# Kernel tuning notes

Hardware: AMD Instinct MI355X
Metric: run time of the kernel (lower is better)

Reference implementation:

```python
import jax, jax.numpy as jnp
import numpy as np

D_IN, D_H, D_OUT = 1024, 1024, 1024
D_MOE = 4096
N_EXPERTS = 8
TOP_K = 2


def setup_inputs() -> dict:
    key = jax.random.key(0)
    ks = jax.random.split(key, 10)
    s = lambda d: 1.0 / np.sqrt(d)
    x = jax.random.normal(ks[0], (2, 2048, D_IN), dtype=jnp.float32)
    W_in = jax.random.normal(ks[1], (D_IN, D_H), dtype=jnp.float32) * s(D_IN)
    b_in = jnp.zeros((D_H,), jnp.float32)
    W_gate = jax.random.normal(ks[2], (D_H, N_EXPERTS), dtype=jnp.float32) * s(D_H)
    b_gate = jnp.zeros((N_EXPERTS,), jnp.float32)
    W1 = jax.random.normal(ks[3], (N_EXPERTS, D_H, D_MOE), dtype=jnp.float32) * s(D_H)
    b1 = jnp.zeros((N_EXPERTS, D_MOE), jnp.float32)
    W2 = jax.random.normal(ks[4], (N_EXPERTS, D_MOE, D_H), dtype=jnp.float32) * s(D_MOE)
    b2 = jnp.zeros((N_EXPERTS, D_H), jnp.float32)
    W_out = jax.random.normal(ks[5], (D_H, D_OUT), dtype=jnp.float32) * s(D_H)
    b_out = jnp.zeros((D_OUT,), jnp.float32)
    return {"x": x, "W_in": W_in, "b_in": b_in, "W_gate": W_gate, "b_gate": b_gate,
            "W1": W1, "b1": b1, "W2": W2, "b2": b2, "W_out": W_out, "b_out": b_out}


def reference(x, W_in, b_in, W_gate, b_gate, W1, b1, W2, b2, W_out, b_out):
    B, S, _ = x.shape
    h = x @ W_in + b_in                       # [B,S,D_H]
    t = h.reshape(B * S, -1)                  # tokens [N,D_H]

    # --- top-k softmax gating ---
    logits = t @ W_gate + b_gate              # [N,E]
    probs = jax.nn.softmax(logits, axis=-1)
    topv, topi = jax.lax.top_k(probs, TOP_K)  # [N,k]
    topv = topv / jnp.sum(topv, axis=-1, keepdims=True)
    # dense routing weights [N,E] (zeros for unselected experts)
    route = jnp.zeros_like(probs).at[jnp.arange(t.shape[0])[:, None], topi].set(topv)

    # --- expert MLPs (dense all-expert compute, weighted combine) ---
    mid = jax.nn.relu(jnp.einsum('nd,edh->neh', t, W1) + b1)   # [N,E,D_MOE]
    eout = jnp.einsum('neh,ehd->ned', mid, W2) + b2            # [N,E,D_H]
    moe_out = jnp.einsum('ne,ned->nd', route, eout)            # [N,D_H]

    out = moe_out.reshape(B, S, -1) @ W_out + b_out            # [B,S,D_OUT]
    return out
```

## Files before the change

kernel.cpp:

```cpp
#include <hip/hip_runtime.h>
#include <hip/hip_bf16.h>

typedef __bf16 bf16_t;
typedef bf16_t bf16x8 __attribute__((ext_vector_type(8)));
typedef bf16_t bf16x4 __attribute__((ext_vector_type(4)));
typedef float f32x4 __attribute__((ext_vector_type(4)));

#define DIN 1024
#define DH 1024
#define DMOE 4096
#define NEXP 8
#define NTOK 4096

__device__ __forceinline__ void gload_lds16(const bf16_t* g, bf16_t* l) {
  __builtin_amdgcn_global_load_lds(
      (const __attribute__((address_space(1))) void*)g,
      (__attribute__((address_space(3))) void*)l, 16, 0, 0);
}

__global__ void k_transpose_all(const float* __restrict__ W_in, const float* __restrict__ W1,
                                const float* __restrict__ W2, const float* __restrict__ W_out,
                                bf16_t* __restrict__ WtIn, bf16_t* __restrict__ Wt1,
                                bf16_t* __restrict__ Wt2, bf16_t* __restrict__ WtOut) {
  const int z = blockIdx.x;
  const float* s; bf16_t* d; int R, C, tx, ty;
  if (z < 256) {
    s = W_in; d = WtIn; R = DIN; C = DH; tx = z & 15; ty = z >> 4;
  } else if (z < 8448) {
    const int l = z - 256, e = l >> 10, t = l & 1023;
    s = W1 + (size_t)e * DH * DMOE; d = Wt1 + (size_t)e * DH * DMOE;
    R = DH; C = DMOE; tx = t & 63; ty = t >> 6;
  } else if (z < 16640) {
    const int l = z - 8448, e = l >> 10, t = l & 1023;
    s = W2 + (size_t)e * DMOE * DH; d = Wt2 + (size_t)e * DMOE * DH;
    R = DMOE; C = DH; tx = t & 15; ty = t >> 4;
  } else {
    const int t = z - 16640;
    s = W_out; d = WtOut; R = DH; C = DH; tx = t & 15; ty = t >> 4;
  }
  __shared__ float tile[64][65];
  const int c0 = tx * 64, r0 = ty * 64;
  const int t = threadIdx.x;
  const int rr = t >> 4;
  const int cc = (t & 15) << 2;
#pragma unroll
  for (int i = 0; i < 64; i += 16) {
    const float4 v = *(const float4*)&s[(size_t)(r0 + rr + i) * C + c0 + cc];
    tile[rr + i][cc + 0] = v.x;
    tile[rr + i][cc + 1] = v.y;
    tile[rr + i][cc + 2] = v.z;
    tile[rr + i][cc + 3] = v.w;
  }
  __syncthreads();
  const int orr = (t & 7) * 8;
  const int oc = t >> 3;
#pragma unroll
  for (int i = 0; i < 64; i += 32) {
    bf16x8 o;
#pragma unroll
    for (int j = 0; j < 8; ++j) o[j] = (bf16_t)tile[orr + j][oc + i];
    *(bf16x8*)&d[(size_t)(c0 + oc + i) * R + r0 + orr] = o;
  }
}

__global__ void k_cvt_bf16(const float* __restrict__ src, bf16_t* __restrict__ dst, int n4) {
  const int i = blockIdx.x * blockDim.x + threadIdx.x;
  if (i < n4) {
    const float4 v = *(const float4*)(src + (size_t)i * 4);
    bf16x4 o;
    o.x = (bf16_t)v.x; o.y = (bf16_t)v.y; o.z = (bf16_t)v.z; o.w = (bf16_t)v.w;
    *(bf16x4*)(dst + (size_t)i * 4) = o;
  }
}

__global__ void k_gate_prep(const float* __restrict__ Win, const float* __restrict__ Wgate,
                            const float* __restrict__ b_in, const float* __restrict__ b_gate,
                            double* __restrict__ G, double* __restrict__ cvec,
                            int* __restrict__ cnt) {
  if (blockIdx.x == 0 && threadIdx.x < 8) cnt[threadIdx.x] = 0;
  const int lane = threadIdx.x & 63;
  const int wave = (blockIdx.x * blockDim.x + threadIdx.x) >> 6;
  const int nw = (gridDim.x * blockDim.x) >> 6;
  for (int d = wave; d <= DIN; d += nw) {
    const float* row = (d < DIN) ? (Win + (size_t)d * DH) : b_in;
    double acc[8] = {0, 0, 0, 0, 0, 0, 0, 0};
    for (int k = lane; k < DH; k += 64) {
      const double xv = (double)row[k];
      const float* g = Wgate + (size_t)k * NEXP;
#pragma unroll
      for (int ee = 0; ee < 8; ++ee) acc[ee] += xv * (double)g[ee];
    }
#pragma unroll
    for (int ee = 0; ee < 8; ++ee) {
      double a = acc[ee];
      for (int o = 32; o > 0; o >>= 1) a += __shfl_down(a, o);
      acc[ee] = a;
    }
    if (lane == 0) {
      if (d < DIN) {
#pragma unroll
        for (int ee = 0; ee < 8; ++ee) G[(size_t)d * 8 + ee] = acc[ee];
      } else {
#pragma unroll
        for (int ee = 0; ee < 8; ++ee) cvec[ee] = acc[ee] + (double)b_gate[ee];
      }
    }
  }
}

__global__ void k_gating(const float* __restrict__ x, const double* __restrict__ G,
                         const double* __restrict__ cvec, int* __restrict__ cnt,
                         int* __restrict__ list, float* __restrict__ wlist) {
  const int lane = threadIdx.x & 63;
  const int t = blockIdx.x * (blockDim.x >> 6) + (threadIdx.x >> 6);
  if (t >= NTOK) return;
  const float* xr = x + (size_t)t * DIN;
  double acc[8] = {0, 0, 0, 0, 0, 0, 0, 0};
  for (int d = lane; d < DIN; d += 64) {
    const double xv = (double)xr[d];
    const double* g = G + (size_t)d * 8;
#pragma unroll
    for (int ee = 0; ee < 8; ++ee) acc[ee] += xv * g[ee];
  }
#pragma unroll
  for (int ee = 0; ee < 8; ++ee) {
    double a = acc[ee];
    for (int o = 32; o > 0; o >>= 1) a += __shfl_down(a, o);
    acc[ee] = a;
  }
  if (lane == 0) {
    double l[8];
#pragma unroll
    for (int ee = 0; ee < 8; ++ee) l[ee] = acc[ee] + cvec[ee];
    double m = l[0];
#pragma unroll
    for (int ee = 1; ee < 8; ++ee) m = fmax(m, l[ee]);
    double p[8];
#pragma unroll
    for (int ee = 0; ee < 8; ++ee) p[ee] = exp(l[ee] - m);
    int i1 = 0;
#pragma unroll
    for (int ee = 1; ee < 8; ++ee)
      if (p[ee] > p[i1]) i1 = ee;
    int i2 = (i1 == 0) ? 1 : 0;
#pragma unroll
    for (int ee = 0; ee < 8; ++ee)
      if (ee != i1 && p[ee] > p[i2]) i2 = ee;
    const double s2 = p[i1] + p[i2];
    const float w1 = (float)(p[i1] / s2);
    const float w2 = (float)(p[i2] / s2);
    int lp = atomicAdd(&cnt[i1], 1);
    list[i1 * NTOK + lp] = t * 2;
    wlist[i1 * NTOK + lp] = w1;
    lp = atomicAdd(&cnt[i2], 1);
    list[i2 * NTOK + lp] = t * 2 + 1;
    wlist[i2 * NTOK + lp] = w2;
  }
}

__global__ void k_scan(const int* __restrict__ cnt, int* __restrict__ offs) {
  if (threadIdx.x == 0) {
    int s = 0;
    for (int e = 0; e < NEXP; ++e) { offs[e] = s; s += cnt[e]; }
    offs[NEXP] = s;
  }
}

__global__ void k_combine(const bf16_t* __restrict__ eout, bf16_t* __restrict__ moebf) {
  const int i = blockIdx.x * blockDim.x + threadIdx.x;
  const int t = i >> 8;
  const int q = (i & 255) * 4;
  const bf16x4 a = *(const bf16x4*)(eout + ((size_t)t * 2) * DH + q);
  const bf16x4 b = *(const bf16x4*)(eout + ((size_t)t * 2 + 1) * DH + q);
  bf16x4 o;
  o.x = (bf16_t)((float)a.x + (float)b.x);
  o.y = (bf16_t)((float)a.y + (float)b.y);
  o.z = (bf16_t)((float)a.z + (float)b.z);
  o.w = (bf16_t)((float)a.w + (float)b.w);
  *(bf16x4*)(moebf + (size_t)t * DH + q) = o;
}

template <int OUT_F32>
__global__ __launch_bounds__(256, 3) void k_gemm_plain(
    const bf16_t* __restrict__ A, const bf16_t* __restrict__ B,
    const float* __restrict__ bias, void* __restrict__ Cbase,
    int M, int N, int K) {
  const int mblk = blockIdx.y, nblk = blockIdx.x;

  __shared__ bf16_t As[3][128 * 32];
  __shared__ bf16_t Bs[3][128 * 32];

  const int tid = threadIdx.x;
  const int lane = tid & 63;
  const int wid = tid >> 6;
  const int wr = wid >> 1, wc = wid & 1;

  const int srow0 = wid * 32 + (lane >> 2);
  const int srow1 = srow0 + 16;
  const int skcol = ((lane & 3) ^ ((lane >> 3) & 3)) * 8;

  const bf16_t* aptr0 = A + (size_t)(mblk * 128 + srow0) * K + skcol;
  const bf16_t* aptr1 = A + (size_t)(mblk * 128 + srow1) * K + skcol;
  const bf16_t* bptr0 = B + (size_t)(nblk * 128 + srow0) * K + skcol;
  const bf16_t* bptr1 = B + (size_t)(nblk * 128 + srow1) * K + skcol;

  const int ldsOfsA0 = (wid * 32) * 32;
  const int ldsOfsA1 = (wid * 32 + 16) * 32;

  f32x4 acc[4][4] = {};
  const int nkt = K >> 5;

  auto stage = [&](int buf, int kt) {
    const size_t ko = (size_t)kt * 32;
    gload_lds16(aptr0 + ko, &As[buf][ldsOfsA0]);
    gload_lds16(aptr1 + ko, &As[buf][ldsOfsA1]);
    gload_lds16(bptr0 + ko, &Bs[buf][ldsOfsA0]);
    gload_lds16(bptr1 + ko, &Bs[buf][ldsOfsA1]);
  };

  stage(0, 0);
  if (nkt > 1) stage(1, 1);

  const int fr = lane & 15;
  const int s0 = (((lane >> 4) ^ ((fr >> 1) & 3)) << 3);

  int cur = 0;
  for (int kt = 0; kt < nkt; ++kt) {
    int nxt = cur + 2;
    if (nxt >= 3) nxt -= 3;
    if (kt + 2 < nkt) {
      stage(nxt, kt + 2);
      asm volatile("s_waitcnt vmcnt(8)" ::: "memory");
    } else if (kt + 1 < nkt) {
      asm volatile("s_waitcnt vmcnt(4)" ::: "memory");
    } else {
      asm volatile("s_waitcnt vmcnt(0)" ::: "memory");
    }
    __builtin_amdgcn_s_barrier();

    bf16x8 af[4], bfr[4];
#pragma unroll
    for (int m = 0; m < 4; ++m)
      af[m] = *(const bf16x8*)&As[cur][(wr * 64 + m * 16 + fr) * 32 + s0];
#pragma unroll
    for (int n = 0; n < 4; ++n)
      bfr[n] = *(const bf16x8*)&Bs[cur][(wc * 64 + n * 16 + fr) * 32 + s0];
#pragma unroll
    for (int m = 0; m < 4; ++m)
#pragma unroll
      for (int n = 0; n < 4; ++n)
        acc[m][n] = __builtin_amdgcn_mfma_f32_16x16x32_bf16(af[m], bfr[n], acc[m][n], 0, 0, 0);

    __builtin_amdgcn_s_barrier();
    cur += 1;
    if (cur >= 3) cur -= 3;
  }

  const int colBase = nblk * 128 + wc * 64 + (lane & 15);
  const int rowBase = mblk * 128 + wr * 64 + ((lane >> 4) << 2);
#pragma unroll
  for (int n = 0; n < 4; ++n) {
    const int c = colBase + n * 16;
    const float bv = bias[c];
#pragma unroll
    for (int m = 0; m < 4; ++m) {
#pragma unroll
      for (int j = 0; j < 4; ++j) {
        const int r = rowBase + m * 16 + j;
        const float v = acc[m][n][j] + bv;
        if constexpr (OUT_F32 == 0) {
          ((bf16_t*)Cbase)[(size_t)r * N + c] = (bf16_t)v;
        } else {
          ((float*)Cbase)[(size_t)r * N + c] = v;
        }
      }
    }
  }
}

template <int MODE>
__global__ __launch_bounds__(512, 4) void k_gemm256(
    const bf16_t* __restrict__ Abase, const bf16_t* __restrict__ Bbase,
    const float* __restrict__ biasBase, bf16_t* __restrict__ Cbase,
    int N, int K,
    const int* __restrict__ cnt, const int* __restrict__ offs,
    const int* __restrict__ listBase, const float* __restrict__ wlistBase) {
  const int e = blockIdx.z;
  const int mblk = blockIdx.y, nblk = blockIdx.x;
  const int Mloc = cnt[e];
  if (mblk * 256 >= Mloc) return;
  const bf16_t* B = Bbase + (size_t)e * N * K;
  const float* bias = biasBase + (size_t)e * N;
  const int* myList = listBase + e * NTOK;
  const float* myW = (MODE == 2) ? (wlistBase + e * NTOK) : nullptr;
  const int rowOff = offs[e];
  const bf16_t* A = (MODE == 2) ? (Abase + (size_t)rowOff * K) : Abase;

  __shared__ bf16_t As[3][256 * 32];
  __shared__ bf16_t Bs[3][128 * 32];

  const int tid = threadIdx.x;
  const int lane = tid & 63;
  const int wid = tid >> 6;
  const int wr = wid >> 1, wc = wid & 1;

  const int subr = lane >> 2;
  const int skcol = ((lane & 3) ^ ((lane >> 3) & 3)) * 8;

  uint32_t aofs[2];
#pragma unroll
  for (int l = 0; l < 2; ++l) {
    int ar = mblk * 256 + (wid * 2 + l) * 16 + subr;
    if (ar > Mloc - 1) ar = Mloc - 1;
    uint32_t arow = (uint32_t)ar;
    if constexpr (MODE == 1) arow = (uint32_t)(myList[ar] >> 1);
    aofs[l] = arow * (uint32_t)K + skcol;
  }
  const uint32_t bofs = (uint32_t)(nblk * 128 + wid * 16 + subr) * (uint32_t)K + skcol;

  f32x4 acc[4][4] = {};
  const int nkt = K >> 5;

  auto stage = [&](int buf, int kt) {
    const uint32_t ko = (uint32_t)kt * 32;
    gload_lds16(A + aofs[0] + ko, &As[buf][(wid * 2 + 0) * 512]);
    gload_lds16(A + aofs[1] + ko, &As[buf][(wid * 2 + 1) * 512]);
    gload_lds16(B + bofs + ko, &Bs[buf][wid * 512]);
  };

  stage(0, 0);
  if (nkt > 1) stage(1, 1);

  const int fr = lane & 15;
  const int s0 = (((lane >> 4) ^ ((fr >> 1) & 3)) << 3);

  int cur = 0;
  for (int kt = 0; kt < nkt; ++kt) {
    int nxt = cur + 2;
    if (nxt >= 3) nxt -= 3;
    if (kt + 2 < nkt) {
      stage(nxt, kt + 2);
      asm volatile("s_waitcnt vmcnt(6)" ::: "memory");
    } else if (kt + 1 < nkt) {
      asm volatile("s_waitcnt vmcnt(3)" ::: "memory");
    } else {
      asm volatile("s_waitcnt vmcnt(0)" ::: "memory");
    }
    __builtin_amdgcn_s_barrier();

    bf16x8 af[4], bfr[4];
#pragma unroll
    for (int m = 0; m < 4; ++m)
      af[m] = *(const bf16x8*)&As[cur][(wr * 64 + m * 16 + fr) * 32 + s0];
#pragma unroll
    for (int n = 0; n < 4; ++n)
      bfr[n] = *(const bf16x8*)&Bs[cur][(wc * 64 + n * 16 + fr) * 32 + s0];
#pragma unroll
    for (int m = 0; m < 4; ++m)
#pragma unroll
      for (int n = 0; n < 4; ++n)
        acc[m][n] = __builtin_amdgcn_mfma_f32_16x16x32_bf16(af[m], bfr[n], acc[m][n], 0, 0, 0);

    __builtin_amdgcn_s_barrier();
    cur += 1;
    if (cur >= 3) cur -= 3;
  }

  const int colBase = nblk * 128 + wc * 64 + (lane & 15);
  const int rowBase = mblk * 256 + wr * 64 + ((lane >> 4) << 2);
#pragma unroll
  for (int n = 0; n < 4; ++n) {
    const int c = colBase + n * 16;
    const float bv = bias[c];
#pragma unroll
    for (int m = 0; m < 4; ++m) {
#pragma unroll
      for (int j = 0; j < 4; ++j) {
        const int r = rowBase + m * 16 + j;
        if (r < Mloc) {
          const float v = acc[m][n][j] + bv;
          if constexpr (MODE == 1) {
            Cbase[(size_t)(rowOff + r) * N + c] = (bf16_t)fmaxf(v, 0.0f);
          } else {
            const int entry = myList[r];
            const float w = myW[r];
            Cbase[(size_t)entry * DH + c] = (bf16_t)(v * w);
          }
        }
      }
    }
  }
}


extern "C" void kernel_launch(void* const* d_in, const int* in_sizes, int n_in,
                              void* d_out, int out_size, void* d_ws, size_t ws_size,
                              hipStream_t stream) {
  const float* x      = (const float*)d_in[0];
  const float* W_in   = (const float*)d_in[1];
  const float* b_in   = (const float*)d_in[2];
  const float* W_gate = (const float*)d_in[3];
  const float* b_gate = (const float*)d_in[4];
  const float* W1     = (const float*)d_in[5];
  const float* b1     = (const float*)d_in[6];
  const float* W2     = (const float*)d_in[7];
  const float* b2     = (const float*)d_in[8];
  const float* W_out  = (const float*)d_in[9];
  const float* b_out  = (const float*)d_in[10];

  char* ws = (char*)d_ws;
  size_t off = 0;
  auto alloc = [&](size_t bytes) -> void* {
    void* p = ws + off;
    off += (bytes + 255) & ~(size_t)255;
    return p;
  };

  bf16_t* WtIn  = (bf16_t*)alloc((size_t)DH * DIN * 2);
  bf16_t* Wt1   = (bf16_t*)alloc((size_t)NEXP * DMOE * DH * 2);
  bf16_t* Wt2   = (bf16_t*)alloc((size_t)NEXP * DH * DMOE * 2);
  bf16_t* WtOut = (bf16_t*)alloc((size_t)DH * DH * 2);
  bf16_t* xbf   = (bf16_t*)alloc((size_t)NTOK * DIN * 2);
  bf16_t* hbf   = (bf16_t*)alloc((size_t)NTOK * DH * 2);
  bf16_t* mid   = (bf16_t*)alloc((size_t)2 * NTOK * DMOE * 2);
  bf16_t* eoutb = (bf16_t*)alloc((size_t)2 * NTOK * DH * 2);
  bf16_t* moebf = (bf16_t*)alloc((size_t)NTOK * DH * 2);
  double* G     = (double*)alloc((size_t)DIN * 8 * 8);
  double* cvec  = (double*)alloc(8 * 8);
  int*    cnt   = (int*)alloc(NEXP * 4);
  int*    offs  = (int*)alloc((NEXP + 1) * 4);
  int*    list  = (int*)alloc((size_t)NEXP * NTOK * 4);
  float*  wlist = (float*)alloc((size_t)NEXP * NTOK * 4);

  k_transpose_all<<<16896, 256, 0, stream>>>(W_in, W1, W2, W_out, WtIn, Wt1, Wt2, WtOut);
  k_cvt_bf16<<<(NTOK * DIN / 4 + 255) / 256, 256, 0, stream>>>(x, xbf, NTOK * DIN / 4);

  k_gate_prep<<<64, 256, 0, stream>>>(W_in, W_gate, b_in, b_gate, G, cvec, cnt);
  k_gating<<<NTOK / 4, 256, 0, stream>>>(x, G, cvec, cnt, list, wlist);
  k_scan<<<1, 64, 0, stream>>>(cnt, offs);

  k_gemm_plain<0><<<dim3(DH / 128, NTOK / 128, 1), 256, 0, stream>>>(
      xbf, WtIn, b_in, hbf, NTOK, DH, DIN);
  k_gemm256<1><<<dim3(DMOE / 128, NTOK / 256, NEXP), 512, 0, stream>>>(
      hbf, Wt1, b1, mid, DMOE, DH, cnt, offs, list, nullptr);
  k_gemm256<2><<<dim3(DH / 128, NTOK / 256, NEXP), 512, 0, stream>>>(
      mid, Wt2, b2, eoutb, DH, DMOE, cnt, offs, list, wlist);
  k_combine<<<NTOK * DH / 4 / 256, 256, 0, stream>>>(eoutb, moebf);
  k_gemm_plain<1><<<dim3(DH / 128, NTOK / 128, 1), 256, 0, stream>>>(
      moebf, WtOut, b_out, (float*)d_out, NTOK, DH, DH);
}
```

Measured before the change: 576.0 us.

## Split-K the second expert GEMM and fold x conversion into transpose kernel

The second expert GEMM (K=4096) is split into two K-halves launched as separate blocks. Each half writes weighted fp32 partial sums to its own buffer, and a combine kernel sums the four partials per token into bf16. This doubles the block count of a GEMM whose grid (8 N-blocks by about 2 M-blocks per expert) underfills the GPU. The fp32 bf16 conversion of x is merged into the weight-transpose kernel as extra blocks to save a launch. The cost is doubled fp32 intermediate traffic and a larger workspace.

Result: no change. 582.6 us (+1.2%).

```diff
diff --git a/kernel.cpp b/kernel.cpp
--- a/kernel.cpp
+++ b/kernel.cpp
@@ -20,9 +20,19 @@
 
 __global__ void k_transpose_all(const float* __restrict__ W_in, const float* __restrict__ W1,
                                 const float* __restrict__ W2, const float* __restrict__ W_out,
+                                const float* __restrict__ x,
                                 bf16_t* __restrict__ WtIn, bf16_t* __restrict__ Wt1,
-                                bf16_t* __restrict__ Wt2, bf16_t* __restrict__ WtOut) {
+                                bf16_t* __restrict__ Wt2, bf16_t* __restrict__ WtOut,
+                                bf16_t* __restrict__ xbf) {
   const int z = blockIdx.x;
+  if (z >= 16896) {
+    const int i = (z - 16896) * 256 + threadIdx.x;
+    const float4 v = *(const float4*)(x + (size_t)i * 4);
+    bf16x4 o;
+    o.x = (bf16_t)v.x; o.y = (bf16_t)v.y; o.z = (bf16_t)v.z; o.w = (bf16_t)v.w;
+    *(bf16x4*)(xbf + (size_t)i * 4) = o;
+    return;
+  }
   const float* s; bf16_t* d; int R, C, tx, ty;
   if (z < 256) {
     s = W_in; d = WtIn; R = DIN; C = DH; tx = z & 15; ty = z >> 4;
@@ -63,16 +73,6 @@
   }
 }
 
-__global__ void k_cvt_bf16(const float* __restrict__ src, bf16_t* __restrict__ dst, int n4) {
-  const int i = blockIdx.x * blockDim.x + threadIdx.x;
-  if (i < n4) {
-    const float4 v = *(const float4*)(src + (size_t)i * 4);
-    bf16x4 o;
-    o.x = (bf16_t)v.x; o.y = (bf16_t)v.y; o.z = (bf16_t)v.z; o.w = (bf16_t)v.w;
-    *(bf16x4*)(dst + (size_t)i * 4) = o;
-  }
-}
-
 __global__ void k_gate_prep(const float* __restrict__ Win, const float* __restrict__ Wgate,
                             const float* __restrict__ b_in, const float* __restrict__ b_gate,
                             double* __restrict__ G, double* __restrict__ cvec,
@@ -166,17 +166,19 @@
   }
 }
 
-__global__ void k_combine(const bf16_t* __restrict__ eout, bf16_t* __restrict__ moebf) {
+__global__ void k_combine4(const float* __restrict__ e32, bf16_t* __restrict__ moebf) {
   const int i = blockIdx.x * blockDim.x + threadIdx.x;
   const int t = i >> 8;
   const int q = (i & 255) * 4;
-  const bf16x4 a = *(const bf16x4*)(eout + ((size_t)t * 2) * DH + q);
-  const bf16x4 b = *(const bf16x4*)(eout + ((size_t)t * 2 + 1) * DH + q);
+  const float4 a = *(const float4*)(e32 + ((size_t)t * 2) * DH + q);
+  const float4 b = *(const float4*)(e32 + ((size_t)t * 2 + 1) * DH + q);
+  const float4 c = *(const float4*)(e32 + ((size_t)(2 * NTOK + t * 2)) * DH + q);
+  const float4 d = *(const float4*)(e32 + ((size_t)(2 * NTOK + t * 2 + 1)) * DH + q);
   bf16x4 o;
-  o.x = (bf16_t)((float)a.x + (float)b.x);
-  o.y = (bf16_t)((float)a.y + (float)b.y);
-  o.z = (bf16_t)((float)a.z + (float)b.z);
-  o.w = (bf16_t)((float)a.w + (float)b.w);
+  o.x = (bf16_t)(a.x + b.x + c.x + d.x);
+  o.y = (bf16_t)(a.y + b.y + c.y + d.y);
+  o.z = (bf16_t)(a.z + b.z + c.z + d.z);
+  o.w = (bf16_t)(a.w + b.w + c.w + d.w);
   *(bf16x4*)(moebf + (size_t)t * DH + q) = o;
 }
 
@@ -278,13 +280,12 @@
   }
 }
 
-template <int MODE>
-__global__ __launch_bounds__(512, 4) void k_gemm256(
+__global__ __launch_bounds__(512, 4) void k_gemm1(
     const bf16_t* __restrict__ Abase, const bf16_t* __restrict__ Bbase,
     const float* __restrict__ biasBase, bf16_t* __restrict__ Cbase,
     int N, int K,
     const int* __restrict__ cnt, const int* __restrict__ offs,
-    const int* __restrict__ listBase, const float* __restrict__ wlistBase) {
+    const int* __restrict__ listBase) {
   const int e = blockIdx.z;
   const int mblk = blockIdx.y, nblk = blockIdx.x;
   const int Mloc = cnt[e];
@@ -292,9 +293,7 @@
   const bf16_t* B = Bbase + (size_t)e * N * K;
   const float* bias = biasBase + (size_t)e * N;
   const int* myList = listBase + e * NTOK;
-  const float* myW = (MODE == 2) ? (wlistBase + e * NTOK) : nullptr;
   const int rowOff = offs[e];
-  const bf16_t* A = (MODE == 2) ? (Abase + (size_t)rowOff * K) : Abase;
 
   __shared__ bf16_t As[3][256 * 32];
   __shared__ bf16_t Bs[3][128 * 32];
@@ -312,9 +311,7 @@
   for (int l = 0; l < 2; ++l) {
     int ar = mblk * 256 + (wid * 2 + l) * 16 + subr;
     if (ar > Mloc - 1) ar = Mloc - 1;
-    uint32_t arow = (uint32_t)ar;
-    if constexpr (MODE == 1) arow = (uint32_t)(myList[ar] >> 1);
-    aofs[l] = arow * (uint32_t)K + skcol;
+    aofs[l] = (uint32_t)(myList[ar] >> 1) * (uint32_t)K + skcol;
   }
   const uint32_t bofs = (uint32_t)(nblk * 128 + wid * 16 + subr) * (uint32_t)K + skcol;
 
@@ -323,8 +320,8 @@
 
   auto stage = [&](int buf, int kt) {
     const uint32_t ko = (uint32_t)kt * 32;
-    gload_lds16(A + aofs[0] + ko, &As[buf][(wid * 2 + 0) * 512]);
-    gload_lds16(A + aofs[1] + ko, &As[buf][(wid * 2 + 1) * 512]);
+    gload_lds16(Abase + aofs[0] + ko, &As[buf][(wid * 2 + 0) * 512]);
+    gload_lds16(Abase + aofs[1] + ko, &As[buf][(wid * 2 + 1) * 512]);
     gload_lds16(B + bofs + ko, &Bs[buf][wid * 512]);
   };
 
@@ -378,14 +375,115 @@
       for (int j = 0; j < 4; ++j) {
         const int r = rowBase + m * 16 + j;
         if (r < Mloc) {
-          const float v = acc[m][n][j] + bv;
-          if constexpr (MODE == 1) {
-            Cbase[(size_t)(rowOff + r) * N + c] = (bf16_t)fmaxf(v, 0.0f);
-          } else {
-            const int entry = myList[r];
-            const float w = myW[r];
-            Cbase[(size_t)entry * DH + c] = (bf16_t)(v * w);
-          }
+          Cbase[(size_t)(rowOff + r) * N + c] = (bf16_t)fmaxf(acc[m][n][j] + bv, 0.0f);
+        }
+      }
+    }
+  }
+}
+
+__global__ __launch_bounds__(512, 4) void k_gemm2s(
+    const bf16_t* __restrict__ Abase, const bf16_t* __restrict__ Bbase,
+    const float* __restrict__ biasBase, float* __restrict__ Cbase,
+    int N, int K,
+    const int* __restrict__ cnt, const int* __restrict__ offs,
+    const int* __restrict__ listBase, const float* __restrict__ wlistBase) {
+  const int e = blockIdx.z >> 1;
+  const int half = blockIdx.z & 1;
+  const int mblk = blockIdx.y, nblk = blockIdx.x;
+  const int Mloc = cnt[e];
+  if (mblk * 256 >= Mloc) return;
+  const bf16_t* B = Bbase + (size_t)e * N * K;
+  const float* bias = biasBase + (size_t)e * N;
+  const int* myList = listBase + e * NTOK;
+  const float* myW = wlistBase + e * NTOK;
+  const bf16_t* A = Abase + (size_t)offs[e] * K;
+
+  __shared__ bf16_t As[3][256 * 32];
+  __shared__ bf16_t Bs[3][128 * 32];
+
+  const int tid = threadIdx.x;
+  const int lane = tid & 63;
+  const int wid = tid >> 6;
+  const int wr = wid >> 1, wc = wid & 1;
+
+  const int subr = lane >> 2;
+  const int skcol = ((lane & 3) ^ ((lane >> 3) & 3)) * 8;
+
+  uint32_t aofs[2];
+#pragma unroll
+  for (int l = 0; l < 2; ++l) {
+    int ar = mblk * 256 + (wid * 2 + l) * 16 + subr;
+    if (ar > Mloc - 1) ar = Mloc - 1;
+    aofs[l] = (uint32_t)ar * (uint32_t)K + skcol;
+  }
+  const uint32_t bofs = (uint32_t)(nblk * 128 + wid * 16 + subr) * (uint32_t)K + skcol;
+  const uint32_t kbase = (uint32_t)half * (uint32_t)(K >> 1);
+
+  f32x4 acc[4][4] = {};
+  const int nkt = K >> 6;
+
+  auto stage = [&](int buf, int kt) {
+    const uint32_t ko = kbase + (uint32_t)kt * 32;
+    gload_lds16(A + aofs[0] + ko, &As[buf][(wid * 2 + 0) * 512]);
+    gload_lds16(A + aofs[1] + ko, &As[buf][(wid * 2 + 1) * 512]);
+    gload_lds16(B + bofs + ko, &Bs[buf][wid * 512]);
+  };
+
+  stage(0, 0);
+  if (nkt > 1) stage(1, 1);
+
+  const int fr = lane & 15;
+  const int s0 = (((lane >> 4) ^ ((fr >> 1) & 3)) << 3);
+
+  int cur = 0;
+  for (int kt = 0; kt < nkt; ++kt) {
+    int nxt = cur + 2;
+    if (nxt >= 3) nxt -= 3;
+    if (kt + 2 < nkt) {
+      stage(nxt, kt + 2);
+      asm volatile("s_waitcnt vmcnt(6)" ::: "memory");
+    } else if (kt + 1 < nkt) {
+      asm volatile("s_waitcnt vmcnt(3)" ::: "memory");
+    } else {
+      asm volatile("s_waitcnt vmcnt(0)" ::: "memory");
+    }
+    __builtin_amdgcn_s_barrier();
+
+    bf16x8 af[4], bfr[4];
+#pragma unroll
+    for (int m = 0; m < 4; ++m)
+      af[m] = *(const bf16x8*)&As[cur][(wr * 64 + m * 16 + fr) * 32 + s0];
+#pragma unroll
+    for (int n = 0; n < 4; ++n)
+      bfr[n] = *(const bf16x8*)&Bs[cur][(wc * 64 + n * 16 + fr) * 32 + s0];
+#pragma unroll
+    for (int m = 0; m < 4; ++m)
+#pragma unroll
+      for (int n = 0; n < 4; ++n)
+        acc[m][n] = __builtin_amdgcn_mfma_f32_16x16x32_bf16(af[m], bfr[n], acc[m][n], 0, 0, 0);
+
+    __builtin_amdgcn_s_barrier();
+    cur += 1;
+    if (cur >= 3) cur -= 3;
+  }
+
+  const int colBase = nblk * 128 + wc * 64 + (lane & 15);
+  const int rowBase = mblk * 256 + wr * 64 + ((lane >> 4) << 2);
+  const size_t outOfs = (size_t)half * 2 * NTOK * DH;
+#pragma unroll
+  for (int n = 0; n < 4; ++n) {
+    const int c = colBase + n * 16;
+    const float bv = half ? 0.0f : bias[c];
+#pragma unroll
+    for (int m = 0; m < 4; ++m) {
+#pragma unroll
+      for (int j = 0; j < 4; ++j) {
+        const int r = rowBase + m * 16 + j;
+        if (r < Mloc) {
+          const int entry = myList[r];
+          const float w = myW[r];
+          Cbase[outOfs + (size_t)entry * DH + c] = (acc[m][n][j] + bv) * w;
         }
       }
     }
@@ -423,7 +521,7 @@
   bf16_t* xbf   = (bf16_t*)alloc((size_t)NTOK * DIN * 2);
   bf16_t* hbf   = (bf16_t*)alloc((size_t)NTOK * DH * 2);
   bf16_t* mid   = (bf16_t*)alloc((size_t)2 * NTOK * DMOE * 2);
-  bf16_t* eoutb = (bf16_t*)alloc((size_t)2 * NTOK * DH * 2);
+  float*  e32   = (float*)alloc((size_t)2 * 2 * NTOK * DH * 4);
   bf16_t* moebf = (bf16_t*)alloc((size_t)NTOK * DH * 2);
   double* G     = (double*)alloc((size_t)DIN * 8 * 8);
   double* cvec  = (double*)alloc(8 * 8);
@@ -432,8 +530,8 @@
   int*    list  = (int*)alloc((size_t)NEXP * NTOK * 4);
   float*  wlist = (float*)alloc((size_t)NEXP * NTOK * 4);
 
-  k_transpose_all<<<16896, 256, 0, stream>>>(W_in, W1, W2, W_out, WtIn, Wt1, Wt2, WtOut);
-  k_cvt_bf16<<<(NTOK * DIN / 4 + 255) / 256, 256, 0, stream>>>(x, xbf, NTOK * DIN / 4);
+  k_transpose_all<<<20992, 256, 0, stream>>>(W_in, W1, W2, W_out, x,
+                                             WtIn, Wt1, Wt2, WtOut, xbf);
 
   k_gate_prep<<<64, 256, 0, stream>>>(W_in, W_gate, b_in, b_gate, G, cvec, cnt);
   k_gating<<<NTOK / 4, 256, 0, stream>>>(x, G, cvec, cnt, list, wlist);
@@ -441,11 +539,11 @@
 
   k_gemm_plain<0><<<dim3(DH / 128, NTOK / 128, 1), 256, 0, stream>>>(
       xbf, WtIn, b_in, hbf, NTOK, DH, DIN);
-  k_gemm256<1><<<dim3(DMOE / 128, NTOK / 256, NEXP), 512, 0, stream>>>(
-      hbf, Wt1, b1, mid, DMOE, DH, cnt, offs, list, nullptr);
-  k_gemm256<2><<<dim3(DH / 128, NTOK / 256, NEXP), 512, 0, stream>>>(
-      mid, Wt2, b2, eoutb, DH, DMOE, cnt, offs, list, wlist);
-  k_combine<<<NTOK * DH / 4 / 256, 256, 0, stream>>>(eoutb, moebf);
+  k_gemm1<<<dim3(DMOE / 128, NTOK / 256, NEXP), 512, 0, stream>>>(
+      hbf, Wt1, b1, mid, DMOE, DH, cnt, offs, list);
+  k_gemm2s<<<dim3(DH / 128, NTOK / 256, NEXP * 2), 512, 0, stream>>>(
+      mid, Wt2, b2, e32, DH, DMOE, cnt, offs, list, wlist);
+  k_combine4<<<NTOK * DH / 4 / 256, 256, 0, stream>>>(e32, moebf);
   k_gemm_plain<1><<<dim3(DH / 128, NTOK / 128, 1), 256, 0, stream>>>(
       moebf, WtOut, b_out, (float*)d_out, NTOK, DH, DH);
 }
```
